# Kernel tuning notes

Hardware: AMD Instinct MI355X
Metric: run time of the kernel (lower is better)

Reference implementation:

```python
import jax, jax.numpy as jnp
import numpy as np

B, T, D, U, P, E = 32, 10, 10, 50, 50, 256
EPS_ATTN = 1e-8
EPS_LN = 1e-5


def _layer_norm(x, w, b):
    mu = jnp.mean(x, axis=-1, keepdims=True)
    var = jnp.mean((x - mu) ** 2, axis=-1, keepdims=True)
    return (x - mu) / jnp.sqrt(var + EPS_LN) * w + b


def setup_inputs() -> dict:
    key = jax.random.key(0)
    ks = jax.random.split(key, 8)
    xavier = float(np.sqrt(2.0 / (E + E)))
    return {
        "Q": jax.random.normal(ks[0], (B, T, U, E), dtype=jnp.float32),
        "K": jax.random.normal(ks[1], (B, D, P, E), dtype=jnp.float32),
        "V": jax.random.normal(ks[2], (B, D, P, E), dtype=jnp.float32),
        "attention_mask": jnp.zeros((B, T, D, U, P), dtype=jnp.float32),
        "W1": jax.random.normal(ks[3], (E, E), dtype=jnp.float32) * xavier,
        "b1": jnp.zeros((E,), dtype=jnp.float32),
        "W2": jax.random.normal(ks[4], (E, E), dtype=jnp.float32) * xavier,
        "b2": jnp.zeros((E,), dtype=jnp.float32),
        "ln1_w": jnp.ones((E,), dtype=jnp.float32),
        "ln1_b": jnp.zeros((E,), dtype=jnp.float32),
        "ln2_w": jnp.ones((E,), dtype=jnp.float32),
        "ln2_b": jnp.zeros((E,), dtype=jnp.float32),
    }


def reference(Q, K, V, attention_mask, W1, b1, W2, b2, ln1_w, ln1_b, ln2_w, ln2_b):
    # dk = max(1.0, emb_dim); scale = sqrt(dk) + eps
    scale = jnp.sqrt(jnp.asarray(float(max(1.0, Q.shape[-1])), dtype=Q.dtype)) + EPS_ATTN
    # (B,T,D,U,P) attention logits
    qk = jnp.einsum("btue,bdpe->btdup", Q, K) / scale + attention_mask
    score = jax.nn.softmax(qk, axis=-1)
    v_att = jnp.einsum("btdup,bdpe->btdue", score, V)  # (B,T,D,U,E)
    x = Q[:, :, None, :, :] + v_att  # broadcast over doc dim
    x = _layer_norm(x, ln1_w, ln1_b)
    ffn = jnp.maximum(x @ W1.T + b1, 0.0) @ W2.T + b2
    return _layer_norm(ffn + x, ln2_w, ln2_b)
```

## Files before the change

kernel.cpp:

```cpp
#include <hip/hip_runtime.h>
#include <math.h>

#define Bsz 32
#define Tt  10
#define Dd  10
#define Uu  50
#define Pp  50
#define Ee  256

typedef __attribute__((ext_vector_type(8))) short bf16x8;
typedef __attribute__((ext_vector_type(4))) float f32x4;

#define STK 264
#define STV 72
#define STS 72

#define OFF_A 0
#define OFF_B 36864
#define OFF_C 46080
#define SMEM_TOT 48128

__device__ __forceinline__ unsigned short f2bf(float f) {
    unsigned u = __builtin_bit_cast(unsigned, f);
    u += 0x7fffu + ((u >> 16) & 1u);
    return (unsigned short)(u >> 16);
}
__device__ __forceinline__ float bf2f(unsigned short h) {
    unsigned u = ((unsigned)h) << 16;
    return __builtin_bit_cast(float, u);
}
__device__ __forceinline__ bf16x8 ldfrag(const unsigned short* p, int stride, int r0, int c0, int lane) {
    return *(const bf16x8*)(p + (size_t)(r0 + (lane & 15)) * stride + c0 + ((lane >> 4) << 3));
}
__device__ __forceinline__ bf16x8 kfrag(const float* __restrict__ Kb, int n, int k0, int lane) {
    int row = n + (lane & 15);
    row = row > 49 ? 49 : row;
    const int col = k0 + ((lane >> 4) << 3);
    const float4 a = *(const float4*)(Kb + (size_t)row * 256 + col);
    const float4 b = *(const float4*)(Kb + (size_t)row * 256 + col + 4);
    bf16x8 r;
    r[0] = (short)f2bf(a.x); r[1] = (short)f2bf(a.y); r[2] = (short)f2bf(a.z); r[3] = (short)f2bf(a.w);
    r[4] = (short)f2bf(b.x); r[5] = (short)f2bf(b.y); r[6] = (short)f2bf(b.z); r[7] = (short)f2bf(b.w);
    return r;
}
__device__ __forceinline__ bf16x8 wfrag(const unsigned short* wbf, const float* wf, int use_ws,
                                        int n, int k0, int lane) {
    const int row = n + (lane & 15);
    const int col = k0 + ((lane >> 4) << 3);
    if (use_ws) {
        return *(const bf16x8*)(wbf + (size_t)row * 256 + col);
    }
    const float4 a = *(const float4*)(wf + (size_t)row * 256 + col);
    const float4 b = *(const float4*)(wf + (size_t)row * 256 + col + 4);
    bf16x8 r;
    r[0] = (short)f2bf(a.x); r[1] = (short)f2bf(a.y); r[2] = (short)f2bf(a.z); r[3] = (short)f2bf(a.w);
    r[4] = (short)f2bf(b.x); r[5] = (short)f2bf(b.y); r[6] = (short)f2bf(b.z); r[7] = (short)f2bf(b.w);
    return r;
}

__global__ void convert_w_kernel(const float* __restrict__ W1, const float* __restrict__ W2,
                                 unsigned short* __restrict__ ws) {
    int i4 = (blockIdx.x * 256 + threadIdx.x) * 4;
    float4 a = *(const float4*)(W1 + i4);
    ushort4 oa; oa.x = f2bf(a.x); oa.y = f2bf(a.y); oa.z = f2bf(a.z); oa.w = f2bf(a.w);
    *(ushort4*)(ws + i4) = oa;
    float4 b = *(const float4*)(W2 + i4);
    ushort4 ob; ob.x = f2bf(b.x); ob.y = f2bf(b.y); ob.z = f2bf(b.z); ob.w = f2bf(b.w);
    *(ushort4*)(ws + 65536 + i4) = ob;
}

__global__ __launch_bounds__(512, 4) void fusion_kernel(
    const float* __restrict__ Q,  const float* __restrict__ K,
    const float* __restrict__ V,  const float* __restrict__ Msk,
    const float* __restrict__ W1, const float* __restrict__ b1,
    const float* __restrict__ W2, const float* __restrict__ b2,
    const float* __restrict__ ln1w, const float* __restrict__ ln1b,
    const float* __restrict__ ln2w, const float* __restrict__ ln2b,
    const unsigned short* __restrict__ wsbf, int use_ws,
    float* __restrict__ out)
{
    __shared__ __align__(16) unsigned char smem[SMEM_TOT];
    unsigned short* sVt  = (unsigned short*)(smem + OFF_A);
    unsigned short* sXbf = (unsigned short*)(smem + OFF_A);
    unsigned short* sH   = (unsigned short*)(smem + OFF_A);
    unsigned short* sS   = (unsigned short*)(smem + OFF_B);
    float*          red  = (float*)(smem + OFF_C);
    float*          red2 = (float*)(smem + OFF_C);

    const int tid  = threadIdx.x;
    const int lane = tid & 63;
    const int wave = tid >> 6;
    const int quad = lane >> 4;
    const int l15  = lane & 15;

    const int btd = ((blockIdx.x & 7) * 400) + (blockIdx.x >> 3);
    const int b   = btd / (Tt * Dd);
    const int rem = btd % (Tt * Dd);
    const int t   = rem / Dd;
    const int d   = rem % Dd;

    const float* Qb = Q + ((size_t)(b * Tt + t) * Uu) * Ee;
    const float* Kb = K + ((size_t)(b * Dd + d) * Pp) * Ee;
    const float* Vb = V + ((size_t)(b * Dd + d) * Pp) * Ee;
    const float* Mb = Msk + ((size_t)((b * Tt + t) * Dd + d) * Uu) * Pp;
    float*       Ob = out + ((size_t)((b * Tt + t) * Dd + d) * Uu) * Ee;

    if (wave < 4) {
        const int mt = wave;
        int arow = mt * 16 + l15; if (arow > 49) arow = 49;
        const float* qrow = Qb + (size_t)arow * Ee + (quad << 3);
        f32x4 acc[4];
        #pragma unroll
        for (int i = 0; i < 4; ++i) acc[i] = (f32x4){0.f, 0.f, 0.f, 0.f};
        #pragma unroll
        for (int k0 = 0; k0 < 256; k0 += 32) {
            float4 qa = *(const float4*)(qrow + k0);
            float4 qb = *(const float4*)(qrow + k0 + 4);
            bf16x8 a;
            a[0] = (short)f2bf(qa.x); a[1] = (short)f2bf(qa.y); a[2] = (short)f2bf(qa.z); a[3] = (short)f2bf(qa.w);
            a[4] = (short)f2bf(qb.x); a[5] = (short)f2bf(qb.y); a[6] = (short)f2bf(qb.z); a[7] = (short)f2bf(qb.w);
            #pragma unroll
            for (int nt = 0; nt < 4; ++nt) {
                bf16x8 bf = kfrag(Kb, nt << 4, k0, lane);
                acc[nt] = __builtin_amdgcn_mfma_f32_16x16x32_bf16(a, bf, acc[nt], 0, 0, 0);
            }
        }
        float l[4][4];
        #pragma unroll
        for (int nt = 0; nt < 4; ++nt) {
            int p = (nt << 4) + l15;
            #pragma unroll
            for (int r = 0; r < 4; ++r) {
                int u = mt * 16 + (quad << 2) + r;
                float v = acc[nt][r] * 0.0625f;
                if (p < Pp) { if (u < Uu) v += Mb[u * Pp + p]; }
                else v = -1e30f;
                l[nt][r] = v;
            }
        }
        #pragma unroll
        for (int r = 0; r < 4; ++r) {
            float m = fmaxf(fmaxf(l[0][r], l[1][r]), fmaxf(l[2][r], l[3][r]));
            #pragma unroll
            for (int msk = 1; msk < 16; msk <<= 1) m = fmaxf(m, __shfl_xor(m, msk));
            float e0 = __expf(l[0][r] - m), e1 = __expf(l[1][r] - m);
            float e2 = __expf(l[2][r] - m), e3 = __expf(l[3][r] - m);
            float s = e0 + e1 + e2 + e3;
            #pragma unroll
            for (int msk = 1; msk < 16; msk <<= 1) s += __shfl_xor(s, msk);
            float inv = 1.0f / s;
            int u = mt * 16 + (quad << 2) + r;
            sS[u * STS +  0 + l15] = f2bf(e0 * inv);
            sS[u * STS + 16 + l15] = f2bf(e1 * inv);
            sS[u * STS + 32 + l15] = f2bf(e2 * inv);
            sS[u * STS + 48 + l15] = f2bf(e3 * inv);
        }
    } else {
        const int lt = tid - 256;
        #pragma unroll 4
        for (int i = lt; i < 12800; i += 256) {
            int p = i >> 8, e = i & 255;
            sVt[e * STV + p] = f2bf(Vb[p * Ee + e]);
        }
        for (int i = lt; i < 3584; i += 256) {
            int p = 50 + (i >> 8), e = i & 255;
            sVt[e * STV + p] = 0;
        }
    }
    __syncthreads();

    {
        const int mt = wave >> 1;
        const int nh = (wave & 1) << 7;
        f32x4 acc[8];
        #pragma unroll
        for (int i = 0; i < 8; ++i) acc[i] = (f32x4){0.f, 0.f, 0.f, 0.f};
        #pragma unroll
        for (int k0 = 0; k0 < 64; k0 += 32) {
            bf16x8 a = ldfrag(sS, STS, mt << 4, k0, lane);
            #pragma unroll
            for (int nt = 0; nt < 8; ++nt) {
                bf16x8 bf = ldfrag(sVt, STV, nh + (nt << 4), k0, lane);
                acc[nt] = __builtin_amdgcn_mfma_f32_16x16x32_bf16(a, bf, acc[nt], 0, 0, 0);
            }
        }
        float s1[4] = {0.f, 0.f, 0.f, 0.f}, s2[4] = {0.f, 0.f, 0.f, 0.f};
        #pragma unroll
        for (int nt = 0; nt < 8; ++nt) {
            int e = nh + (nt << 4) + l15;
            #pragma unroll
            for (int r = 0; r < 4; ++r) {
                int u = (mt << 4) + (quad << 2) + r;
                float x = 0.f;
                if (u < Uu) x = acc[nt][r] + Qb[(size_t)u * Ee + e];
                acc[nt][r] = x;
                s1[r] += x; s2[r] += x * x;
            }
        }
        #pragma unroll
        for (int msk = 1; msk < 16; msk <<= 1) {
            #pragma unroll
            for (int r = 0; r < 4; ++r) { s1[r] += __shfl_xor(s1[r], msk); s2[r] += __shfl_xor(s2[r], msk); }
        }
        if (l15 == 0) {
            #pragma unroll
            for (int r = 0; r < 4; ++r) {
                int u = (mt << 4) + (quad << 2) + r;
                red[u * 4 + (wave & 1) * 2 + 0] = s1[r];
                red[u * 4 + (wave & 1) * 2 + 1] = s2[r];
            }
        }
        __syncthreads();
        float mu[4], rstd[4];
        #pragma unroll
        for (int r = 0; r < 4; ++r) {
            int u = (mt << 4) + (quad << 2) + r;
            float sum = red[u * 4 + 0] + red[u * 4 + 2];
            float sq  = red[u * 4 + 1] + red[u * 4 + 3];
            mu[r] = sum * (1.0f / 256.0f);
            float var = sq * (1.0f / 256.0f) - mu[r] * mu[r];
            rstd[r] = rsqrtf(var + 1e-5f);
        }
        #pragma unroll
        for (int nt = 0; nt < 8; ++nt) {
            int e = nh + (nt << 4) + l15;
            float wv = ln1w[e], bv = ln1b[e];
            #pragma unroll
            for (int r = 0; r < 4; ++r) {
                int u = (mt << 4) + (quad << 2) + r;
                float o = (u < Uu) ? ((acc[nt][r] - mu[r]) * rstd[r] * wv + bv) : 0.f;
                sXbf[u * STK + e] = f2bf(o);
            }
        }
    }
    __syncthreads();

    const int mp = wave >> 2;
    const int nq = wave & 3;
    unsigned resid[2][4][2];
    {
        f32x4 acc2[2][4];
        #pragma unroll
        for (int mi = 0; mi < 2; ++mi)
            #pragma unroll
            for (int nt = 0; nt < 4; ++nt) acc2[mi][nt] = (f32x4){0.f, 0.f, 0.f, 0.f};
        float b1v[4];
        #pragma unroll
        for (int nt = 0; nt < 4; ++nt) b1v[nt] = b1[(nq << 6) + (nt << 4) + l15];
        #pragma unroll
        for (int k0 = 0; k0 < 256; k0 += 32) {
            bf16x8 a0 = ldfrag(sXbf, STK, (mp << 5),      k0, lane);
            bf16x8 a1 = ldfrag(sXbf, STK, (mp << 5) + 16, k0, lane);
            #pragma unroll
            for (int nt = 0; nt < 4; ++nt) {
                bf16x8 bf = wfrag(wsbf, W1, use_ws, (nq << 6) + (nt << 4), k0, lane);
                acc2[0][nt] = __builtin_amdgcn_mfma_f32_16x16x32_bf16(a0, bf, acc2[0][nt], 0, 0, 0);
                acc2[1][nt] = __builtin_amdgcn_mfma_f32_16x16x32_bf16(a1, bf, acc2[1][nt], 0, 0, 0);
            }
        }
        #pragma unroll
        for (int mi = 0; mi < 2; ++mi)
            #pragma unroll
            for (int nt = 0; nt < 4; ++nt) {
                int j = (nq << 6) + (nt << 4) + l15;
                #pragma unroll
                for (int rp = 0; rp < 2; ++rp) {
                    int u0 = (mp << 5) + (mi << 4) + (quad << 2) + rp * 2;
                    unsigned lo = sXbf[(size_t)u0 * STK + j];
                    unsigned hi = sXbf[(size_t)(u0 + 1) * STK + j];
                    resid[mi][nt][rp] = lo | (hi << 16);
                }
            }
        __syncthreads();
        #pragma unroll
        for (int mi = 0; mi < 2; ++mi)
            #pragma unroll
            for (int nt = 0; nt < 4; ++nt) {
                int j = (nq << 6) + (nt << 4) + l15;
                #pragma unroll
                for (int r = 0; r < 4; ++r) {
                    int u = (mp << 5) + (mi << 4) + (quad << 2) + r;
                    sH[u * STK + j] = f2bf(fmaxf(acc2[mi][nt][r] + b1v[nt], 0.f));
                }
            }
    }
    __syncthreads();

    {
        f32x4 acc2[2][4];
        #pragma unroll
        for (int mi = 0; mi < 2; ++mi)
            #pragma unroll
            for (int nt = 0; nt < 4; ++nt) acc2[mi][nt] = (f32x4){0.f, 0.f, 0.f, 0.f};
        float b2v[4], w2l[4], b2l[4];
        #pragma unroll
        for (int nt = 0; nt < 4; ++nt) {
            int j = (nq << 6) + (nt << 4) + l15;
            b2v[nt] = b2[j]; w2l[nt] = ln2w[j]; b2l[nt] = ln2b[j];
        }
        #pragma unroll
        for (int k0 = 0; k0 < 256; k0 += 32) {
            bf16x8 a0 = ldfrag(sH, STK, (mp << 5),      k0, lane);
            bf16x8 a1 = ldfrag(sH, STK, (mp << 5) + 16, k0, lane);
            #pragma unroll
            for (int nt = 0; nt < 4; ++nt) {
                bf16x8 bf = wfrag(wsbf + 65536, W2, use_ws, (nq << 6) + (nt << 4), k0, lane);
                acc2[0][nt] = __builtin_amdgcn_mfma_f32_16x16x32_bf16(a0, bf, acc2[0][nt], 0, 0, 0);
                acc2[1][nt] = __builtin_amdgcn_mfma_f32_16x16x32_bf16(a1, bf, acc2[1][nt], 0, 0, 0);
            }
        }
        float s1[2][4], s2[2][4];
        #pragma unroll
        for (int mi = 0; mi < 2; ++mi)
            #pragma unroll
            for (int r = 0; r < 4; ++r) { s1[mi][r] = 0.f; s2[mi][r] = 0.f; }
        #pragma unroll
        for (int mi = 0; mi < 2; ++mi)
            #pragma unroll
            for (int nt = 0; nt < 4; ++nt) {
                #pragma unroll
                for (int r = 0; r < 4; ++r) {
                    unsigned pk = resid[mi][nt][r >> 1];
                    unsigned short rb = (r & 1) ? (unsigned short)(pk >> 16) : (unsigned short)(pk & 0xffffu);
                    float y = acc2[mi][nt][r] + b2v[nt] + bf2f(rb);
                    acc2[mi][nt][r] = y;
                    s1[mi][r] += y; s2[mi][r] += y * y;
                }
            }
        #pragma unroll
        for (int msk = 1; msk < 16; msk <<= 1)
            #pragma unroll
            for (int mi = 0; mi < 2; ++mi)
                #pragma unroll
                for (int r = 0; r < 4; ++r) {
                    s1[mi][r] += __shfl_xor(s1[mi][r], msk);
                    s2[mi][r] += __shfl_xor(s2[mi][r], msk);
                }
        if (l15 == 0) {
            #pragma unroll
            for (int mi = 0; mi < 2; ++mi)
                #pragma unroll
                for (int r = 0; r < 4; ++r) {
                    int u = (mp << 5) + (mi << 4) + (quad << 2) + r;
                    red2[u * 8 + nq * 2 + 0] = s1[mi][r];
                    red2[u * 8 + nq * 2 + 1] = s2[mi][r];
                }
        }
        __syncthreads();
        #pragma unroll
        for (int mi = 0; mi < 2; ++mi)
            #pragma unroll
            for (int r = 0; r < 4; ++r) {
                int u = (mp << 5) + (mi << 4) + (quad << 2) + r;
                if (u < Uu) {
                    float sum = red2[u * 8 + 0] + red2[u * 8 + 2] + red2[u * 8 + 4] + red2[u * 8 + 6];
                    float sq  = red2[u * 8 + 1] + red2[u * 8 + 3] + red2[u * 8 + 5] + red2[u * 8 + 7];
                    float mu = sum * (1.0f / 256.0f);
                    float var = sq * (1.0f / 256.0f) - mu * mu;
                    float rstd = rsqrtf(var + 1e-5f);
                    #pragma unroll
                    for (int nt = 0; nt < 4; ++nt) {
                        int j = (nq << 6) + (nt << 4) + l15;
                        Ob[(size_t)u * Ee + j] = (acc2[mi][nt][r] - mu) * rstd * w2l[nt] + b2l[nt];
                    }
                }
            }
    }
}

extern "C" void kernel_launch(void* const* d_in, const int* in_sizes, int n_in,
                              void* d_out, int out_size, void* d_ws, size_t ws_size,
                              hipStream_t stream) {
    const float* Q    = (const float*)d_in[0];
    const float* K    = (const float*)d_in[1];
    const float* V    = (const float*)d_in[2];
    const float* M    = (const float*)d_in[3];
    const float* W1   = (const float*)d_in[4];
    const float* b1   = (const float*)d_in[5];
    const float* W2   = (const float*)d_in[6];
    const float* b2   = (const float*)d_in[7];
    const float* ln1w = (const float*)d_in[8];
    const float* ln1b = (const float*)d_in[9];
    const float* ln2w = (const float*)d_in[10];
    const float* ln2b = (const float*)d_in[11];
    float* out = (float*)d_out;

    int use_ws = (ws_size >= 262144) ? 1 : 0;
    const unsigned short* wsbf = (const unsigned short*)d_ws;
    if (use_ws) {
        convert_w_kernel<<<64, 256, 0, stream>>>(W1, W2, (unsigned short*)d_ws);
    }
    fusion_kernel<<<Bsz * Tt * Dd, 512, 0, stream>>>(Q, K, V, M, W1, b1, W2, b2,
                                                     ln1w, ln1b, ln2w, ln2b,
                                                     wsbf, use_ws, out);
}
```

Measured before the change: 588.9 us.

## Split fused attention+FFN kernel into separate attention and FFN kernels

Splits the single fused kernel into two. The attention kernel writes the LayerNorm1 output as fp32 to the output buffer in global memory. The FFN kernel reads it back from there for the first GEMM operand and for the residual. This lowers per-kernel shared memory and register pressure, which could raise occupancy. The cost is an extra global round trip of the 50x256 fp32 activation per block, about 400 MB total, plus an extra launch. The residual is now kept in fp32 rather than bf16, which slightly changes precision.

Result: slower. 673.9 us (+14.4%).

```diff
diff --git a/kernel.cpp b/kernel.cpp
--- a/kernel.cpp
+++ b/kernel.cpp
@@ -11,14 +11,18 @@
 typedef __attribute__((ext_vector_type(8))) short bf16x8;
 typedef __attribute__((ext_vector_type(4))) float f32x4;
 
-#define STK 264
+#define STH 264
 #define STV 72
 #define STS 72
 
-#define OFF_A 0
-#define OFF_B 36864
-#define OFF_C 46080
-#define SMEM_TOT 48128
+#define K1_OFF_V 0
+#define K1_OFF_S 36864
+#define K1_OFF_R 46080
+#define K1_SMEM  47104
+
+#define K2_OFF_H 0
+#define K2_OFF_R 33792
+#define K2_SMEM  35840
 
 __device__ __forceinline__ unsigned short f2bf(float f) {
     unsigned u = __builtin_bit_cast(unsigned, f);
@@ -32,12 +36,12 @@
 __device__ __forceinline__ bf16x8 ldfrag(const unsigned short* p, int stride, int r0, int c0, int lane) {
     return *(const bf16x8*)(p + (size_t)(r0 + (lane & 15)) * stride + c0 + ((lane >> 4) << 3));
 }
-__device__ __forceinline__ bf16x8 kfrag(const float* __restrict__ Kb, int n, int k0, int lane) {
+__device__ __forceinline__ bf16x8 gfrag49(const float* __restrict__ base, int n, int k0, int lane) {
     int row = n + (lane & 15);
     row = row > 49 ? 49 : row;
     const int col = k0 + ((lane >> 4) << 3);
-    const float4 a = *(const float4*)(Kb + (size_t)row * 256 + col);
-    const float4 b = *(const float4*)(Kb + (size_t)row * 256 + col + 4);
+    const float4 a = *(const float4*)(base + (size_t)row * 256 + col);
+    const float4 b = *(const float4*)(base + (size_t)row * 256 + col + 4);
     bf16x8 r;
     r[0] = (short)f2bf(a.x); r[1] = (short)f2bf(a.y); r[2] = (short)f2bf(a.z); r[3] = (short)f2bf(a.w);
     r[4] = (short)f2bf(b.x); r[5] = (short)f2bf(b.y); r[6] = (short)f2bf(b.z); r[7] = (short)f2bf(b.w);
@@ -69,23 +73,16 @@
     *(ushort4*)(ws + 65536 + i4) = ob;
 }
 
-__global__ __launch_bounds__(512, 4) void fusion_kernel(
+__global__ __launch_bounds__(512, 4) void attn_kernel(
     const float* __restrict__ Q,  const float* __restrict__ K,
     const float* __restrict__ V,  const float* __restrict__ Msk,
-    const float* __restrict__ W1, const float* __restrict__ b1,
-    const float* __restrict__ W2, const float* __restrict__ b2,
     const float* __restrict__ ln1w, const float* __restrict__ ln1b,
-    const float* __restrict__ ln2w, const float* __restrict__ ln2b,
-    const unsigned short* __restrict__ wsbf, int use_ws,
     float* __restrict__ out)
 {
-    __shared__ __align__(16) unsigned char smem[SMEM_TOT];
-    unsigned short* sVt  = (unsigned short*)(smem + OFF_A);
-    unsigned short* sXbf = (unsigned short*)(smem + OFF_A);
-    unsigned short* sH   = (unsigned short*)(smem + OFF_A);
-    unsigned short* sS   = (unsigned short*)(smem + OFF_B);
-    float*          red  = (float*)(smem + OFF_C);
-    float*          red2 = (float*)(smem + OFF_C);
+    __shared__ __align__(16) unsigned char smem[K1_SMEM];
+    unsigned short* sVt = (unsigned short*)(smem + K1_OFF_V);
+    unsigned short* sS  = (unsigned short*)(smem + K1_OFF_S);
+    float*          red = (float*)(smem + K1_OFF_R);
 
     const int tid  = threadIdx.x;
     const int lane = tid & 63;
@@ -103,7 +100,7 @@
     const float* Kb = K + ((size_t)(b * Dd + d) * Pp) * Ee;
     const float* Vb = V + ((size_t)(b * Dd + d) * Pp) * Ee;
     const float* Mb = Msk + ((size_t)((b * Tt + t) * Dd + d) * Uu) * Pp;
-    float*       Ob = out + ((size_t)((b * Tt + t) * Dd + d) * Uu) * Ee;
+    float*       Xb = out + ((size_t)btd * Uu) * Ee;
 
     if (wave < 4) {
         const int mt = wave;
@@ -121,7 +118,7 @@
             a[4] = (short)f2bf(qb.x); a[5] = (short)f2bf(qb.y); a[6] = (short)f2bf(qb.z); a[7] = (short)f2bf(qb.w);
             #pragma unroll
             for (int nt = 0; nt < 4; ++nt) {
-                bf16x8 bf = kfrag(Kb, nt << 4, k0, lane);
+                bf16x8 bf = gfrag49(Kb, nt << 4, k0, lane);
                 acc[nt] = __builtin_amdgcn_mfma_f32_16x16x32_bf16(a, bf, acc[nt], 0, 0, 0);
             }
         }
@@ -211,33 +208,49 @@
             }
         }
         __syncthreads();
-        float mu[4], rstd[4];
         #pragma unroll
         for (int r = 0; r < 4; ++r) {
             int u = (mt << 4) + (quad << 2) + r;
-            float sum = red[u * 4 + 0] + red[u * 4 + 2];
-            float sq  = red[u * 4 + 1] + red[u * 4 + 3];
-            mu[r] = sum * (1.0f / 256.0f);
-            float var = sq * (1.0f / 256.0f) - mu[r] * mu[r];
-            rstd[r] = rsqrtf(var + 1e-5f);
-        }
-        #pragma unroll
-        for (int nt = 0; nt < 8; ++nt) {
-            int e = nh + (nt << 4) + l15;
-            float wv = ln1w[e], bv = ln1b[e];
-            #pragma unroll
-            for (int r = 0; r < 4; ++r) {
-                int u = (mt << 4) + (quad << 2) + r;
-                float o = (u < Uu) ? ((acc[nt][r] - mu[r]) * rstd[r] * wv + bv) : 0.f;
-                sXbf[u * STK + e] = f2bf(o);
-            }
-        }
-    }
-    __syncthreads();
+            if (u < Uu) {
+                float sum = red[u * 4 + 0] + red[u * 4 + 2];
+                float sq  = red[u * 4 + 1] + red[u * 4 + 3];
+                float mu = sum * (1.0f / 256.0f);
+                float var = sq * (1.0f / 256.0f) - mu * mu;
+                float rstd = rsqrtf(var + 1e-5f);
+                #pragma unroll
+                for (int nt = 0; nt < 8; ++nt) {
+                    int e = nh + (nt << 4) + l15;
+                    Xb[(size_t)u * Ee + e] = (acc[nt][r] - mu) * rstd * ln1w[e] + ln1b[e];
+                }
+            }
+        }
+    }
+}
+
+__global__ __launch_bounds__(512, 4) void ffn_kernel(
+    const float* __restrict__ W1, const float* __restrict__ b1,
+    const float* __restrict__ W2, const float* __restrict__ b2,
+    const float* __restrict__ ln2w, const float* __restrict__ ln2b,
+    const unsigned short* __restrict__ wsbf, int use_ws,
+    float* __restrict__ out)
+{
+    __shared__ __align__(16) unsigned char smem[K2_SMEM];
+    unsigned short* sH   = (unsigned short*)(smem + K2_OFF_H);
+    float*          red2 = (float*)(smem + K2_OFF_R);
+
+    const int tid  = threadIdx.x;
+    const int lane = tid & 63;
+    const int wave = tid >> 6;
+    const int quad = lane >> 4;
+    const int l15  = lane & 15;
+
+    const int btd = blockIdx.x;
+    const float* Xb = out + (size_t)btd * Uu * Ee;
+    float*       Ob = out + (size_t)btd * Uu * Ee;
 
     const int mp = wave >> 2;
     const int nq = wave & 3;
-    unsigned resid[2][4][2];
+
     {
         f32x4 acc2[2][4];
         #pragma unroll
@@ -249,8 +262,8 @@
         for (int nt = 0; nt < 4; ++nt) b1v[nt] = b1[(nq << 6) + (nt << 4) + l15];
         #pragma unroll
         for (int k0 = 0; k0 < 256; k0 += 32) {
-            bf16x8 a0 = ldfrag(sXbf, STK, (mp << 5),      k0, lane);
-            bf16x8 a1 = ldfrag(sXbf, STK, (mp << 5) + 16, k0, lane);
+            bf16x8 a0 = gfrag49(Xb, (mp << 5),      k0, lane);
+            bf16x8 a1 = gfrag49(Xb, (mp << 5) + 16, k0, lane);
             #pragma unroll
             for (int nt = 0; nt < 4; ++nt) {
                 bf16x8 bf = wfrag(wsbf, W1, use_ws, (nq << 6) + (nt << 4), k0, lane);
@@ -264,23 +277,9 @@
             for (int nt = 0; nt < 4; ++nt) {
                 int j = (nq << 6) + (nt << 4) + l15;
                 #pragma unroll
-                for (int rp = 0; rp < 2; ++rp) {
-                    int u0 = (mp << 5) + (mi << 4) + (quad << 2) + rp * 2;
-                    unsigned lo = sXbf[(size_t)u0 * STK + j];
-                    unsigned hi = sXbf[(size_t)(u0 + 1) * STK + j];
-                    resid[mi][nt][rp] = lo | (hi << 16);
-                }
-            }
-        __syncthreads();
-        #pragma unroll
-        for (int mi = 0; mi < 2; ++mi)
-            #pragma unroll
-            for (int nt = 0; nt < 4; ++nt) {
-                int j = (nq << 6) + (nt << 4) + l15;
-                #pragma unroll
                 for (int r = 0; r < 4; ++r) {
                     int u = (mp << 5) + (mi << 4) + (quad << 2) + r;
-                    sH[u * STK + j] = f2bf(fmaxf(acc2[mi][nt][r] + b1v[nt], 0.f));
+                    sH[u * STH + j] = f2bf(fmaxf(acc2[mi][nt][r] + b1v[nt], 0.f));
                 }
             }
     }
@@ -300,8 +299,8 @@
         }
         #pragma unroll
         for (int k0 = 0; k0 < 256; k0 += 32) {
-            bf16x8 a0 = ldfrag(sH, STK, (mp << 5),      k0, lane);
-            bf16x8 a1 = ldfrag(sH, STK, (mp << 5) + 16, k0, lane);
+            bf16x8 a0 = ldfrag(sH, STH, (mp << 5),      k0, lane);
+            bf16x8 a1 = ldfrag(sH, STH, (mp << 5) + 16, k0, lane);
             #pragma unroll
             for (int nt = 0; nt < 4; ++nt) {
                 bf16x8 bf = wfrag(wsbf + 65536, W2, use_ws, (nq << 6) + (nt << 4), k0, lane);
@@ -318,11 +317,12 @@
         for (int mi = 0; mi < 2; ++mi)
             #pragma unroll
             for (int nt = 0; nt < 4; ++nt) {
+                int j = (nq << 6) + (nt << 4) + l15;
                 #pragma unroll
                 for (int r = 0; r < 4; ++r) {
-                    unsigned pk = resid[mi][nt][r >> 1];
-                    unsigned short rb = (r & 1) ? (unsigned short)(pk >> 16) : (unsigned short)(pk & 0xffffu);
-                    float y = acc2[mi][nt][r] + b2v[nt] + bf2f(rb);
+                    int u = (mp << 5) + (mi << 4) + (quad << 2) + r;
+                    float xr = (u < Uu) ? Xb[(size_t)u * Ee + j] : 0.f;
+                    float y = acc2[mi][nt][r] + b2v[nt] + xr;
                     acc2[mi][nt][r] = y;
                     s1[mi][r] += y; s2[mi][r] += y * y;
                 }
@@ -390,7 +390,7 @@
     if (use_ws) {
         convert_w_kernel<<<64, 256, 0, stream>>>(W1, W2, (unsigned short*)d_ws);
     }
-    fusion_kernel<<<Bsz * Tt * Dd, 512, 0, stream>>>(Q, K, V, M, W1, b1, W2, b2,
-                                                     ln1w, ln1b, ln2w, ln2b,
-                                                     wsbf, use_ws, out);
-}
+    attn_kernel<<<Bsz * Tt * Dd, 512, 0, stream>>>(Q, K, V, M, ln1w, ln1b, out);
+    ffn_kernel<<<Bsz * Tt * Dd, 512, 0, stream>>>(W1, b1, W2, b2, ln2w, ln2b,
+                                                  wsbf, use_ws, out);
+}
```
